# Kernel optimization log

Measured on AMD Instinct MI355X. Metric: run time of the kernel, lower is better.

## Reference

```python
import jax, jax.numpy as jnp
import numpy as np

N = 10000      # nodes
E = 160000     # edges (avg degree 16)
DIN = 512      # in_channels
H = 512        # hidden_channels
OUT = 128      # out_channels
L = 3          # num_layers
EPS_LN = 1e-5


def _ln(x):
    # F.layer_norm over last dim, no learned affine
    m = jnp.mean(x, axis=-1, keepdims=True)
    v = jnp.mean((x - m) ** 2, axis=-1, keepdims=True)
    return (x - m) * jax.lax.rsqrt(v + EPS_LN)


def setup_inputs() -> dict:
    key = jax.random.key(0)
    ks = jax.random.split(key, 16)
    s = 0.02
    return {
        "x": jax.random.normal(ks[0], (N, DIN), jnp.float32),
        "edge_index": jax.random.randint(ks[1], (2, E), 0, N, dtype=jnp.int64),
        "W_in": jax.random.normal(ks[2], (DIN, H), jnp.float32) * s,
        "b_in": jnp.zeros((H,), jnp.float32),
        "Wq": jax.random.normal(ks[3], (L, H, H), jnp.float32) * s,
        "Wk": jax.random.normal(ks[4], (L, H, H), jnp.float32) * s,
        "Wv": jax.random.normal(ks[5], (L, H, H), jnp.float32) * s,
        "Wo": jax.random.normal(ks[6], (L, H, H), jnp.float32) * s,
        "bo": jnp.zeros((L, H), jnp.float32),
        "W_gcn": jax.random.normal(ks[7], (H, H), jnp.float32) * s,
        "b_gcn": jnp.zeros((H,), jnp.float32),
        "W_mix": jax.random.normal(ks[8], (2 * H, H), jnp.float32) * s,
        "b_mix": jnp.zeros((H,), jnp.float32),
        "W_cls": jax.random.normal(ks[9], (H, OUT), jnp.float32) * s,
        "b_cls": jnp.zeros((OUT,), jnp.float32),
    }


def _attn_layer(x, wq, wk, wv, wo, bo):
    q = jax.nn.elu(x @ wq) + 1.0               # [N,H], positive feature map
    k = jax.nn.elu(x @ wk) + 1.0               # [N,H]
    v = x @ wv                                  # [N,H]
    kv = k.T @ v                                # [H,H]
    z = 1.0 / jnp.maximum(q @ k.sum(axis=0), 1e-6)   # [N]
    h = (q @ kv) * z[:, None]                   # [N,H]
    return h @ wo + bo


def _gcn(x, edge_index, w, b):
    # PyG GCNConv: x@W, add self-loops, symmetric D^-1/2 (A+I) D^-1/2, +bias
    xw = x @ w
    n = xw.shape[0]
    loops = jnp.arange(n, dtype=edge_index.dtype)
    src = jnp.concatenate([edge_index[0], loops])
    dst = jnp.concatenate([edge_index[1], loops])
    deg = jax.ops.segment_sum(jnp.ones_like(dst, jnp.float32), dst, num_segments=n)
    dis = jnp.where(deg > 0, jax.lax.rsqrt(jnp.maximum(deg, 1e-12)), 0.0)
    norm = dis[src] * dis[dst]                  # [E+N]
    msg = xw[src] * norm[:, None]               # [E+N,H]
    return jax.ops.segment_sum(msg, dst, num_segments=n) + b


def reference(x, edge_index, W_in, b_in, Wq, Wk, Wv, Wo, bo,
              W_gcn, b_gcn, W_mix, b_mix, W_cls, b_cls):
    # eval mode: dropout is identity
    x0 = jax.nn.relu(x @ W_in + b_in)           # [N,H]
    h_global = x0
    for i in range(Wq.shape[0]):
        h = _attn_layer(h_global, Wq[i], Wk[i], Wv[i], Wo[i], bo[i])
        h_global = _ln(h_global + h)
    h_graph = jax.nn.relu(_gcn(x0, edge_index, W_gcn, b_gcn))
    h = jax.nn.relu(jnp.concatenate([h_global, h_graph], axis=-1) @ W_mix + b_mix)
    return h @ W_cls + b_cls                    # [N,OUT]
```

## Files before the change

kernel.cpp:

```cpp
#include <hip/hip_runtime.h>
#include <hip/hip_bf16.h>

#define NNODES 10000
#define EEDGES 160000
#define HD     512
#define OUTD   128
#define NLAYERS 3
#define MP     10112
#define KTP    10240

#define ACT_NONE 0
#define ACT_RELU 1
#define ACT_ELU1 2

typedef __attribute__((ext_vector_type(8))) short bf16x8;
typedef __attribute__((ext_vector_type(4))) float f32x4;

__device__ __forceinline__ void gload16(const void* g, void* l) {
  __builtin_amdgcn_global_load_lds(
      (const __attribute__((address_space(1))) void*)g,
      (__attribute__((address_space(3))) void*)l, 16, 0, 0);
}

__device__ __forceinline__ void unp8(uint4 v, float* f) {
  const ushort* u = (const ushort*)&v;
#pragma unroll
  for (int j = 0; j < 8; ++j) f[j] = __uint_as_float(((unsigned)u[j]) << 16);
}

__device__ __forceinline__ ushort f2bu(float f) {
  __hip_bfloat16 h = __float2bfloat16(f);
  return *reinterpret_cast<ushort*>(&h);
}

__device__ __forceinline__ float elu1f(float v) {
  return (v > 0.f) ? (v + 1.0f) : __expf(v);
}

__global__ void fill_f32(float* p, float v, int n) {
  int i = blockIdx.x * blockDim.x + threadIdx.x;
  if (i < n) p[i] = v;
}
__global__ void fill_i32(int* p, int v, int n) {
  int i = blockIdx.x * blockDim.x + threadIdx.x;
  if (i < n) p[i] = v;
}

__global__ void probe_i64_k(const void* ei, int* flag, int E_) {
  int i = blockIdx.x * blockDim.x + threadIdx.x;
  if (i < E_) {
    if (((const int*)ei)[2 * i + 1] != 0) atomicOr(flag, 1);
  }
}
__device__ inline void load_edge(const void* ei, int is_i32, int e, int E_, int& s, int& d) {
  if (is_i32) { s = ((const int*)ei)[e]; d = ((const int*)ei)[E_ + e]; }
  else { s = (int)((const long long*)ei)[e]; d = (int)((const long long*)ei)[E_ + e]; }
}

template<int ACT, int HAS_BIAS, int HAS_SCALE, int OUTF, int OUTB, int ATOMIC, int TQKV>
__global__ __launch_bounds__(256) void mgemm(
    const __hip_bfloat16* __restrict__ A, const __hip_bfloat16* __restrict__ Bt,
    const float* __restrict__ bias, const float* __restrict__ rowscale,
    float* __restrict__ Cf, __hip_bfloat16* __restrict__ Cb,
    __hip_bfloat16* __restrict__ kTp, __hip_bfloat16* __restrict__ vTp,
    int M, int lda, int ldb, int ldc, int ldcb, int Ksz)
{
  __shared__ __align__(16) __hip_bfloat16 As[128 * 32];
  __shared__ __align__(16) __hip_bfloat16 Bs[128 * 32];
  __shared__ __align__(16) ushort eps[TQKV ? 128 * 136 : 8];

  int nwg = gridDim.x * gridDim.y;
  int orig = blockIdx.y * gridDim.x + blockIdx.x;
  int qq = nwg >> 3, rr8 = nwg & 7;
  int xcd = orig & 7, idx = orig >> 3;
  int wg = (xcd < rr8 ? xcd * (qq + 1) : rr8 * (qq + 1) + (xcd - rr8) * qq) + idx;
  int bx = wg % gridDim.x, by = wg / gridDim.x;

  int tid = threadIdx.x;
  int lane = tid & 63;
  int wave = tid >> 6;
  int wm = wave >> 1, wn = wave & 1;
  int row0 = by * 128;
  int col0 = bx * 128;
  int koff = blockIdx.z * Ksz;
  int srow = lane >> 2;
  int sbyte = (lane & 3) * 16;

  f32x4 acc[4][4];
#pragma unroll
  for (int i = 0; i < 4; ++i)
#pragma unroll
    for (int j = 0; j < 4; ++j) acc[i][j] = f32x4{0.f, 0.f, 0.f, 0.f};

  int r16 = lane & 15;
  int kg = (lane >> 4) * 16;

  for (int k0 = koff; k0 < koff + Ksz; k0 += 32) {
#pragma unroll
    for (int j = 0; j < 2; ++j) {
      int c = wave * 2 + j;
      const char* ga = (const char*)(A + (long)(row0 + c * 16 + srow) * lda + k0) + sbyte;
      gload16(ga, (char*)As + c * 1024);
      const char* gb = (const char*)(Bt + (long)(col0 + c * 16 + srow) * ldb + k0) + sbyte;
      gload16(gb, (char*)Bs + c * 1024);
    }
    __syncthreads();
    bf16x8 af[4], bfr[4];
#pragma unroll
    for (int i = 0; i < 4; ++i)
      af[i] = *(const bf16x8*)((const char*)As + (wm * 64 + i * 16 + r16) * 64 + kg);
#pragma unroll
    for (int i = 0; i < 4; ++i)
      bfr[i] = *(const bf16x8*)((const char*)Bs + (wn * 64 + i * 16 + r16) * 64 + kg);
#pragma unroll
    for (int i = 0; i < 4; ++i)
#pragma unroll
      for (int j = 0; j < 4; ++j)
        acc[i][j] = __builtin_amdgcn_mfma_f32_16x16x32_bf16(af[i], bfr[j], acc[i][j], 0, 0, 0);
    __syncthreads();
  }

  int rg = (lane >> 4) * 4;
  if (TQKV) {
    int colg = col0 + wn * 64;
    int g = colg >> 9;
    int cbase = col0 & 511;
#pragma unroll
    for (int i = 0; i < 4; ++i) {
#pragma unroll
      for (int j = 0; j < 4; ++j) {
        int c_l = wn * 64 + j * 16 + r16;
        int row_l = wm * 64 + i * 16 + rg;
        if (g == 0) {
#pragma unroll
          for (int r = 0; r < 4; ++r)
            eps[(row_l + r) * 136 + c_l] = f2bu(elu1f(acc[i][j][r]));
        } else {
          ushort4 o;
          o.x = f2bu(g == 1 ? elu1f(acc[i][j][0]) : acc[i][j][0]);
          o.y = f2bu(g == 1 ? elu1f(acc[i][j][1]) : acc[i][j][1]);
          o.z = f2bu(g == 1 ? elu1f(acc[i][j][2]) : acc[i][j][2]);
          o.w = f2bu(g == 1 ? elu1f(acc[i][j][3]) : acc[i][j][3]);
          *(ushort4*)&eps[c_l * 136 + row_l] = o;
        }
      }
    }
    __syncthreads();
    int l16 = tid & 15, cw = tid >> 4;
    if (g == 0) {
#pragma unroll
      for (int rr = cw; rr < 128; rr += 16) {
        int node = row0 + rr;
        if (node < NNODES)
          *(uint4*)((ushort*)Cb + (long)node * ldcb + cbase + l16 * 8) =
              *(const uint4*)&eps[rr * 136 + l16 * 8];
      }
    } else {
      ushort* T = (ushort*)(g == 1 ? kTp : vTp);
      int node0 = row0 + l16 * 8;
      if (node0 < NNODES) {
#pragma unroll
        for (int cc = cw; cc < 128; cc += 16)
          *(uint4*)(T + (long)(cbase + cc) * KTP + node0) = *(const uint4*)&eps[cc * 136 + l16 * 8];
      }
    }
    return;
  }
#pragma unroll
  for (int i = 0; i < 4; ++i) {
#pragma unroll
    for (int j = 0; j < 4; ++j) {
      int col = col0 + wn * 64 + j * 16 + r16;
#pragma unroll
      for (int r = 0; r < 4; ++r) {
        int row = row0 + wm * 64 + i * 16 + rg + r;
        if (row >= M) continue;
        float v = acc[i][j][r];
        if (ATOMIC) { atomicAdd(&Cf[(long)row * ldc + col], v); continue; }
        if (HAS_SCALE) v *= rowscale[row];
        if (HAS_BIAS) v += bias[col];
        if (ACT == ACT_RELU) v = fmaxf(v, 0.f);
        if (ACT == ACT_ELU1) v = elu1f(v);
        if (OUTF) Cf[(long)row * ldc + col] = v;
        if (OUTB) Cb[(long)row * ldcb + col] = __float2bfloat16(v);
      }
    }
  }
}

__global__ __launch_bounds__(256) void wtrans_k(
    const float* W_in, const float* Wq, const float* Wk, const float* Wv,
    const float* Wo, const float* W_gcn, const float* W_mix,
    __hip_bfloat16* WT, __hip_bfloat16* WMT)
{
  int z = blockIdx.z;
  const float* src;
  __hip_bfloat16* out;
  int ldout = 512, koff = 0;
  if (z == 0) { src = W_in; out = WT; }
  else if (z <= 9) {
    int l = (z - 1) / 3, w = (z - 1) % 3;
    src = (w == 0 ? Wq : w == 1 ? Wk : Wv) + (long)l * 262144;
    out = WT + (long)z * 262144;
  } else if (z <= 12) { src = Wo + (long)(z - 10) * 262144; out = WT + (long)z * 262144; }
  else if (z == 13) { src = W_gcn; out = WT + 13L * 262144; }
  else { src = W_mix + (long)(z - 14) * 262144; out = WMT; ldout = 1024; koff = (z - 14) * 512; }
  __shared__ float t[32][33];
  int r0 = blockIdx.y * 32, c0 = blockIdx.x * 32;
  int tx = threadIdx.x & 31, ty = threadIdx.x >> 5;
#pragma unroll
  for (int i = 0; i < 32; i += 8) t[ty + i][tx] = src[(long)(r0 + ty + i) * 512 + c0 + tx];
  __syncthreads();
#pragma unroll
  for (int i = 0; i < 32; i += 8)
    out[(long)(c0 + ty + i) * ldout + koff + r0 + tx] = __float2bfloat16(t[tx][ty + i]);
}

__global__ __launch_bounds__(256) void wtrans_cls_k(const float* Wc, __hip_bfloat16* out) {
  __shared__ float t[32][33];
  int r0 = blockIdx.y * 32, c0 = blockIdx.x * 32;
  int tx = threadIdx.x & 31, ty = threadIdx.x >> 5;
#pragma unroll
  for (int i = 0; i < 32; i += 8) t[ty + i][tx] = Wc[(long)(r0 + ty + i) * 128 + c0 + tx];
  __syncthreads();
#pragma unroll
  for (int i = 0; i < 32; i += 8)
    out[(long)(c0 + ty + i) * 512 + r0 + tx] = __float2bfloat16(t[tx][ty + i]);
}

__global__ void castx_k(const float* __restrict__ x, __hip_bfloat16* __restrict__ xb) {
  long i = (long)blockIdx.x * 256 + threadIdx.x;
  long base = i * 8;
  if (base >= (long)MP * HD) return;
  int row = (int)(base >> 9);
  ushort o[8];
  if (row < NNODES) {
    float4 a = *(const float4*)(x + base);
    float4 b = *(const float4*)(x + base + 4);
    float f[8] = {a.x, a.y, a.z, a.w, b.x, b.y, b.z, b.w};
#pragma unroll
    for (int j = 0; j < 8; ++j) o[j] = f2bu(f[j]);
  } else {
#pragma unroll
    for (int j = 0; j < 8; ++j) o[j] = 0;
  }
  *(uint4*)((ushort*)xb + base) = *(const uint4*)o;
}

__global__ __launch_bounds__(256) void pzcs_k(__hip_bfloat16* kT, __hip_bfloat16* vT,
                                              float* __restrict__ ksum) {
  int i = (blockIdx.x * 256 + threadIdx.x) >> 6;
  int lane = threadIdx.x & 63;
  ushort* kr = (ushort*)kT + (long)i * KTP;
  ushort* vr = (ushort*)vT + (long)i * KTP;
  if (lane < 60) {
    ushort4 z4 = {0, 0, 0, 0};
    *(ushort4*)(kr + NNODES + lane * 4) = z4;
    *(ushort4*)(vr + NNODES + lane * 4) = z4;
  }
  float s = 0.f;
  for (int off = lane * 8; off < NNODES; off += 512) {
    uint4 v = *(const uint4*)(kr + off);
    float f[8]; unp8(v, f);
#pragma unroll
    for (int j = 0; j < 8; ++j) s += f[j];
  }
#pragma unroll
  for (int o = 32; o > 0; o >>= 1) s += __shfl_down(s, o);
  if (lane == 0) ksum[i] = s;
}

__global__ __launch_bounds__(256) void z_k(const __hip_bfloat16* __restrict__ qb,
                                           const float* __restrict__ ksum, float* __restrict__ z) {
  long gid = (long)blockIdx.x * 256 + threadIdx.x;
  int row = (int)(gid >> 6), lane = (int)(gid & 63);
  if (row >= NNODES) return;
  uint4 qv = *(const uint4*)((const ushort*)qb + (long)row * HD + lane * 8);
  float f[8]; unp8(qv, f);
  const float* kk = ksum + lane * 8;
  float s = 0.f;
#pragma unroll
  for (int j = 0; j < 8; ++j) s += f[j] * kk[j];
#pragma unroll
  for (int o = 32; o > 0; o >>= 1) s += __shfl_down(s, o);
  if (lane == 0) z[row] = 1.0f / fmaxf(s, 1e-6f);
}

__global__ void cast8_k(const float* __restrict__ s, __hip_bfloat16* __restrict__ d, int n8) {
  int i = blockIdx.x * 256 + threadIdx.x;
  if (i >= n8) return;
  float4 a = ((const float4*)s)[2 * i], b = ((const float4*)s)[2 * i + 1];
  float f[8] = {a.x, a.y, a.z, a.w, b.x, b.y, b.z, b.w};
  ushort o[8];
#pragma unroll
  for (int j = 0; j < 8; ++j) o[j] = f2bu(f[j]);
  *(uint4*)((ushort*)d + (long)i * 8) = *(const uint4*)o;
}

__global__ __launch_bounds__(256) void ln_res_k(float* __restrict__ hg,
                                                const __hip_bfloat16* __restrict__ hb,
                                                __hip_bfloat16* __restrict__ hgcat) {
  int wid = (blockIdx.x * 256 + threadIdx.x) >> 6;
  int lane = threadIdx.x & 63;
  if (wid >= NNODES) return;
  float* row = hg + (long)wid * HD + lane * 8;
  uint4 hv = *(const uint4*)((const ushort*)hb + (long)wid * HD + lane * 8);
  float hf[8]; unp8(hv, hf);
  float4 p0 = *(const float4*)row, p1 = *(const float4*)(row + 4);
  float a[8] = {p0.x + hf[0], p0.y + hf[1], p0.z + hf[2], p0.w + hf[3],
                p1.x + hf[4], p1.y + hf[5], p1.z + hf[6], p1.w + hf[7]};
  float s = 0.f;
#pragma unroll
  for (int j = 0; j < 8; ++j) s += a[j];
#pragma unroll
  for (int o = 1; o < 64; o <<= 1) s += __shfl_xor(s, o);
  float mean = s * (1.0f / HD);
  float vs = 0.f;
#pragma unroll
  for (int j = 0; j < 8; ++j) { a[j] -= mean; vs += a[j] * a[j]; }
#pragma unroll
  for (int o = 1; o < 64; o <<= 1) vs += __shfl_xor(vs, o);
  float inv = rsqrtf(vs * (1.0f / HD) + 1e-5f);
  ushort ob[8];
#pragma unroll
  for (int j = 0; j < 8; ++j) { a[j] *= inv; ob[j] = f2bu(a[j]); }
  *(float4*)row = make_float4(a[0], a[1], a[2], a[3]);
  *(float4*)(row + 4) = make_float4(a[4], a[5], a[6], a[7]);
  *(uint4*)((ushort*)hgcat + (long)wid * 1024 + lane * 8) = *(const uint4*)ob;
}

__global__ void cnt_k(const void* ei, const int* flag, int* cnt, int E_) {
  int e = blockIdx.x * blockDim.x + threadIdx.x;
  if (e >= E_) return;
  int s, d; load_edge(ei, *flag, e, E_, s, d);
  atomicAdd(&cnt[d], 1);
}
__global__ __launch_bounds__(256) void scan_k(const int* __restrict__ cnt, int* __restrict__ rowptr,
                                              int* __restrict__ cursor, float* __restrict__ dis) {
  __shared__ int ps[256];
  int t = threadIdx.x;
  int lo = t * 40, hi = min(lo + 40, NNODES);
  int s = 0;
  for (int i = lo; i < hi; ++i) s += cnt[i];
  ps[t] = s;
  __syncthreads();
  for (int o = 1; o < 256; o <<= 1) {
    int v = (t >= o) ? ps[t - o] : 0;
    __syncthreads();
    ps[t] += v;
    __syncthreads();
  }
  int run = (t == 0) ? 0 : ps[t - 1];
  for (int i = lo; i < hi; ++i) {
    rowptr[i] = run; cursor[i] = run;
    dis[i] = rsqrtf((float)cnt[i] + 1.0f);
    run += cnt[i];
  }
  if (t == 255) rowptr[NNODES] = run;
}
__global__ void csrfill_k(const void* ei, const int* flag, int* cursor, int* csr, int E_) {
  int e = blockIdx.x * blockDim.x + threadIdx.x;
  if (e >= E_) return;
  int s, d; load_edge(ei, *flag, e, E_, s, d);
  int pos = atomicAdd(&cursor[d], 1);
  csr[pos] = s;
}
__global__ __launch_bounds__(256) void gcn_gather_k(
    const __hip_bfloat16* __restrict__ xwb, const int* __restrict__ rowptr,
    const int* __restrict__ csr, const float* __restrict__ dis,
    const float* __restrict__ bgcn, __hip_bfloat16* __restrict__ hgcat)
{
  int wid = (blockIdx.x * 256 + threadIdx.x) >> 6;
  int lane = threadIdx.x & 63;
  if (wid >= NNODES) return;
  int d = wid;
  float dd = dis[d];
  float acc[8], f[8];
  uint4 v = *(const uint4*)((const ushort*)xwb + (long)d * HD + lane * 8);
  unp8(v, f);
#pragma unroll
  for (int j = 0; j < 8; ++j) acc[j] = f[j] * dd * dd;
  int e0 = rowptr[d], e1 = rowptr[d + 1];
  for (int e = e0; e < e1; ++e) {
    int sN = csr[e];
    float w = dis[sN] * dd;
    uint4 xv = *(const uint4*)((const ushort*)xwb + (long)sN * HD + lane * 8);
    unp8(xv, f);
#pragma unroll
    for (int j = 0; j < 8; ++j) acc[j] = fmaf(f[j], w, acc[j]);
  }
  const float* bb = bgcn + lane * 8;
  ushort o[8];
#pragma unroll
  for (int j = 0; j < 8; ++j) o[j] = f2bu(fmaxf(acc[j] + bb[j], 0.f));
  *(uint4*)((ushort*)hgcat + (long)d * 1024 + 512 + lane * 8) = *(const uint4*)o;
}

extern "C" void kernel_launch(void* const* d_in, const int* in_sizes, int n_in,
                              void* d_out, int out_size, void* d_ws, size_t ws_size,
                              hipStream_t stream) {
  const float* x     = (const float*)d_in[0];
  const void*  ei    = d_in[1];
  const float* W_in  = (const float*)d_in[2];
  const float* b_in  = (const float*)d_in[3];
  const float* Wq    = (const float*)d_in[4];
  const float* Wk    = (const float*)d_in[5];
  const float* Wv    = (const float*)d_in[6];
  const float* Wo    = (const float*)d_in[7];
  const float* bo    = (const float*)d_in[8];
  const float* W_gcn = (const float*)d_in[9];
  const float* b_gcn = (const float*)d_in[10];
  const float* W_mix = (const float*)d_in[11];
  const float* b_mix = (const float*)d_in[12];
  const float* W_cls = (const float*)d_in[13];
  const float* b_cls = (const float*)d_in[14];
  float* out = (float*)d_out;

  char* p = (char*)d_ws;
  __hip_bfloat16* WT  = (__hip_bfloat16*)p; p += 14L * 262144 * 2;
  __hip_bfloat16* WMT = (__hip_bfloat16*)p; p += 512L * 1024 * 2;
  __hip_bfloat16* WCT = (__hip_bfloat16*)p; p += 128L * 512 * 2;
  float* hg = (float*)p; p += (long)MP * HD * 4;
  __hip_bfloat16* hgcat = (__hip_bfloat16*)p; p += (long)MP * 1024 * 2;
  __hip_bfloat16* qb = (__hip_bfloat16*)p; p += (long)MP * HD * 2;
  __hip_bfloat16* vT = (__hip_bfloat16*)p; p += 512L * KTP * 2;
  __hip_bfloat16* kT = (__hip_bfloat16*)p; p += 512L * KTP * 2;
  float* kvf = (float*)p; p += 512L * 512 * 4;
  __hip_bfloat16* kvb  = (__hip_bfloat16*)p; p += 512L * 512 * 2;
  __hip_bfloat16* kvoT = (__hip_bfloat16*)p; p += 512L * 512 * 2;
  float* ksum = (float*)p; p += 2048;
  float* zb   = (float*)p; p += (long)MP * 4;
  int* cnt    = (int*)p; p += 40000;
  int* rowptr = (int*)p; p += 40016;
  int* cursor = (int*)p; p += 40000;
  float* dis  = (float*)p; p += 40000;
  int* csr    = (int*)p; p += 640000;
  int* flag   = (int*)p; p += 4;

  __hip_bfloat16* xb    = qb;
  __hip_bfloat16* xwb   = qb;
  __hip_bfloat16* hb    = kT;
  __hip_bfloat16* hmixb = kT;

  dim3 blk(256);
  dim3 gG(4, MP / 128);
  dim3 gQKV(12, MP / 128);
  dim3 gKV(4, 4, 16);
  dim3 gS(4, 4);
  dim3 gCls(1, MP / 128);

  wtrans_k<<<dim3(16, 16, 16), blk, 0, stream>>>(W_in, Wq, Wk, Wv, Wo, W_gcn, W_mix, WT, WMT);
  wtrans_cls_k<<<dim3(4, 16), blk, 0, stream>>>(W_cls, WCT);
  castx_k<<<(int)(((long)MP * HD / 8 + 255) / 256), blk, 0, stream>>>(x, xb);
  fill_i32<<<1, 1, 0, stream>>>(flag, 0, 1);
  probe_i64_k<<<(EEDGES + 255) / 256, 256, 0, stream>>>(ei, flag, EEDGES);

  mgemm<ACT_RELU, 1, 0, 1, 1, 0, 0><<<gG, blk, 0, stream>>>(
      xb, WT, b_in, nullptr, hg, hgcat, nullptr, nullptr, NNODES, HD, HD, HD, 1024, HD);

  mgemm<ACT_NONE, 0, 0, 0, 1, 0, 0><<<gG, blk, 0, stream>>>(
      hgcat, WT + 13L * 262144, nullptr, nullptr, nullptr, xwb, nullptr, nullptr,
      NNODES, 1024, HD, HD, HD, HD);
  fill_i32<<<40, 256, 0, stream>>>(cnt, 0, NNODES);
  cnt_k<<<(EEDGES + 255) / 256, 256, 0, stream>>>(ei, flag, cnt, EEDGES);
  scan_k<<<1, 256, 0, stream>>>(cnt, rowptr, cursor, dis);
  csrfill_k<<<(EEDGES + 255) / 256, 256, 0, stream>>>(ei, flag, cursor, csr, EEDGES);
  gcn_gather_k<<<2500, blk, 0, stream>>>(xwb, rowptr, csr, dis, b_gcn, hgcat);

  for (int l = 0; l < NLAYERS; ++l) {
    const __hip_bfloat16* BtQKV = WT + (long)(1 + 3 * l) * 262144;
    const __hip_bfloat16* WoT   = WT + (long)(10 + l) * 262144;

    mgemm<ACT_NONE, 0, 0, 0, 0, 0, 1><<<gQKV, blk, 0, stream>>>(
        hgcat, BtQKV, nullptr, nullptr, nullptr, qb, kT, vT,
        NNODES, 1024, HD, HD, HD, HD);
    pzcs_k<<<128, blk, 0, stream>>>(kT, vT, ksum);

    fill_f32<<<1024, 256, 0, stream>>>(kvf, 0.f, HD * HD);
    mgemm<ACT_NONE, 0, 0, 0, 0, 1, 0><<<gKV, blk, 0, stream>>>(
        kT, vT, nullptr, nullptr, kvf, nullptr, nullptr, nullptr,
        HD, KTP, KTP, HD, HD, 640);
    cast8_k<<<128, blk, 0, stream>>>(kvf, kvb, HD * HD / 8);

    mgemm<ACT_NONE, 0, 0, 0, 1, 0, 0><<<gS, blk, 0, stream>>>(
        WoT, kvb, nullptr, nullptr, nullptr, kvoT, nullptr, nullptr,
        HD, HD, HD, HD, HD, HD);

    z_k<<<2500, blk, 0, stream>>>(qb, ksum, zb);
    mgemm<ACT_NONE, 1, 1, 0, 1, 0, 0><<<gG, blk, 0, stream>>>(
        qb, kvoT, bo + (long)l * HD, zb, nullptr, hb, nullptr, nullptr,
        NNODES, HD, HD, HD, HD, HD);
    ln_res_k<<<2500, blk, 0, stream>>>(hg, hb, hgcat);
  }

  mgemm<ACT_RELU, 1, 0, 0, 1, 0, 0><<<gG, blk, 0, stream>>>(
      hgcat, WMT, b_mix, nullptr, nullptr, hmixb, nullptr, nullptr,
      NNODES, 1024, 1024, HD, HD, 1024);
  mgemm<ACT_NONE, 1, 0, 1, 0, 0, 0><<<gCls, blk, 0, stream>>>(
      hmixb, WCT, b_cls, nullptr, out, nullptr, nullptr, nullptr,
      NNODES, HD, HD, OUTD, OUTD, HD);
}
```

Baseline: 731.0 us.

## Fuse init fills, column-sum k in QKV epilogue, merge weight transposes

Replaces the separate fill kernels with one init kernel that zeroes per-layer kv accumulators, ksum, counts, flag and the kT/vT padding up front. The column sum of k is now computed in the QKV GEMM epilogue with wave shuffles and atomics, which removes the per-layer pzcs kernel and its reread of kT. It also folds the W_cls transpose into wtrans_k, uses a ballot in the int64 probe to cut atomics, and unrolls the GCN gather by two edges. Together these remove several launches and memory passes, at the cost of atomics in the GEMM epilogue and an accumulation order that is no longer deterministic.

Result: faster. 703.3 us (-3.8%).

```diff
diff --git a/kernel.cpp b/kernel.cpp
--- a/kernel.cpp
+++ b/kernel.cpp
@@ -37,20 +37,32 @@
   return (v > 0.f) ? (v + 1.0f) : __expf(v);
 }
 
-__global__ void fill_f32(float* p, float v, int n) {
-  int i = blockIdx.x * blockDim.x + threadIdx.x;
-  if (i < n) p[i] = v;
-}
-__global__ void fill_i32(int* p, int v, int n) {
-  int i = blockIdx.x * blockDim.x + threadIdx.x;
-  if (i < n) p[i] = v;
+__global__ __launch_bounds__(256) void init_k(int* cnt, int* flag, float* ksum,
+                                              float* kvf, __hip_bfloat16* kT,
+                                              __hip_bfloat16* vT) {
+  int i = blockIdx.x * 256 + threadIdx.x;
+  if (i < 3 * HD * HD) { kvf[i] = 0.f; return; }
+  i -= 3 * HD * HD;
+  if (i < NNODES) { cnt[i] = 0; return; }
+  i -= NNODES;
+  if (i < 3 * HD) { ksum[i] = 0.f; return; }
+  i -= 3 * HD;
+  if (i == 0) { *flag = 0; return; }
+  i -= 1;
+  if (i < 512 * 120 * 2) {
+    int b = i / (512 * 120);
+    int r = (i % (512 * 120)) / 120;
+    int c = (i % 120);
+    uint* T = (uint*)(b == 0 ? kT : vT);
+    T[((long)r * KTP + NNODES) / 2 + c] = 0u;
+  }
 }
 
 __global__ void probe_i64_k(const void* ei, int* flag, int E_) {
   int i = blockIdx.x * blockDim.x + threadIdx.x;
-  if (i < E_) {
-    if (((const int*)ei)[2 * i + 1] != 0) atomicOr(flag, 1);
-  }
+  bool nz = (i < E_) && (((const int*)ei)[2 * i + 1] != 0);
+  unsigned long long m = __ballot(nz);
+  if ((threadIdx.x & 63) == 0 && m) atomicOr(flag, 1);
 }
 __device__ inline void load_edge(const void* ei, int is_i32, int e, int E_, int& s, int& d) {
   if (is_i32) { s = ((const int*)ei)[e]; d = ((const int*)ei)[E_ + e]; }
@@ -125,6 +137,24 @@
     int colg = col0 + wn * 64;
     int g = colg >> 9;
     int cbase = col0 & 511;
+    if (g == 1) {
+#pragma unroll
+      for (int j = 0; j < 4; ++j) {
+        float cs = 0.f;
+#pragma unroll
+        for (int i = 0; i < 4; ++i) {
+          int rowbase = row0 + wm * 64 + i * 16 + rg;
+          if (rowbase < NNODES) {
+#pragma unroll
+            for (int r = 0; r < 4; ++r) cs += elu1f(acc[i][j][r]);
+          }
+        }
+        cs += __shfl_xor(cs, 16);
+        cs += __shfl_xor(cs, 32);
+        if ((lane >> 4) == 0)
+          atomicAdd(&Cf[cbase + wn * 64 + j * 16 + r16], cs);
+      }
+    }
 #pragma unroll
     for (int i = 0; i < 4; ++i) {
 #pragma unroll
@@ -190,13 +220,13 @@
 
 __global__ __launch_bounds__(256) void wtrans_k(
     const float* W_in, const float* Wq, const float* Wk, const float* Wv,
-    const float* Wo, const float* W_gcn, const float* W_mix,
-    __hip_bfloat16* WT, __hip_bfloat16* WMT)
+    const float* Wo, const float* W_gcn, const float* W_mix, const float* W_cls,
+    __hip_bfloat16* WT, __hip_bfloat16* WMT, __hip_bfloat16* WCT)
 {
   int z = blockIdx.z;
   const float* src;
   __hip_bfloat16* out;
-  int ldout = 512, koff = 0;
+  int ldout = 512, koff = 0, ldsrc = 512;
   if (z == 0) { src = W_in; out = WT; }
   else if (z <= 9) {
     int l = (z - 1) / 3, w = (z - 1) % 3;
@@ -204,28 +234,20 @@
     out = WT + (long)z * 262144;
   } else if (z <= 12) { src = Wo + (long)(z - 10) * 262144; out = WT + (long)z * 262144; }
   else if (z == 13) { src = W_gcn; out = WT + 13L * 262144; }
-  else { src = W_mix + (long)(z - 14) * 262144; out = WMT; ldout = 1024; koff = (z - 14) * 512; }
+  else if (z <= 15) { src = W_mix + (long)(z - 14) * 262144; out = WMT; ldout = 1024; koff = (z - 14) * 512; }
+  else {
+    if (blockIdx.x >= 4) return;
+    src = W_cls; out = WCT; ldsrc = 128;
+  }
   __shared__ float t[32][33];
   int r0 = blockIdx.y * 32, c0 = blockIdx.x * 32;
   int tx = threadIdx.x & 31, ty = threadIdx.x >> 5;
 #pragma unroll
-  for (int i = 0; i < 32; i += 8) t[ty + i][tx] = src[(long)(r0 + ty + i) * 512 + c0 + tx];
+  for (int i = 0; i < 32; i += 8) t[ty + i][tx] = src[(long)(r0 + ty + i) * ldsrc + c0 + tx];
   __syncthreads();
 #pragma unroll
   for (int i = 0; i < 32; i += 8)
     out[(long)(c0 + ty + i) * ldout + koff + r0 + tx] = __float2bfloat16(t[tx][ty + i]);
-}
-
-__global__ __launch_bounds__(256) void wtrans_cls_k(const float* Wc, __hip_bfloat16* out) {
-  __shared__ float t[32][33];
-  int r0 = blockIdx.y * 32, c0 = blockIdx.x * 32;
-  int tx = threadIdx.x & 31, ty = threadIdx.x >> 5;
-#pragma unroll
-  for (int i = 0; i < 32; i += 8) t[ty + i][tx] = Wc[(long)(r0 + ty + i) * 128 + c0 + tx];
-  __syncthreads();
-#pragma unroll
-  for (int i = 0; i < 32; i += 8)
-    out[(long)(c0 + ty + i) * 512 + r0 + tx] = __float2bfloat16(t[tx][ty + i]);
 }
 
 __global__ void castx_k(const float* __restrict__ x, __hip_bfloat16* __restrict__ xb) {
@@ -245,29 +267,6 @@
     for (int j = 0; j < 8; ++j) o[j] = 0;
   }
   *(uint4*)((ushort*)xb + base) = *(const uint4*)o;
-}
-
-__global__ __launch_bounds__(256) void pzcs_k(__hip_bfloat16* kT, __hip_bfloat16* vT,
-                                              float* __restrict__ ksum) {
-  int i = (blockIdx.x * 256 + threadIdx.x) >> 6;
-  int lane = threadIdx.x & 63;
-  ushort* kr = (ushort*)kT + (long)i * KTP;
-  ushort* vr = (ushort*)vT + (long)i * KTP;
-  if (lane < 60) {
-    ushort4 z4 = {0, 0, 0, 0};
-    *(ushort4*)(kr + NNODES + lane * 4) = z4;
-    *(ushort4*)(vr + NNODES + lane * 4) = z4;
-  }
-  float s = 0.f;
-  for (int off = lane * 8; off < NNODES; off += 512) {
-    uint4 v = *(const uint4*)(kr + off);
-    float f[8]; unp8(v, f);
-#pragma unroll
-    for (int j = 0; j < 8; ++j) s += f[j];
-  }
-#pragma unroll
-  for (int o = 32; o > 0; o >>= 1) s += __shfl_down(s, o);
-  if (lane == 0) ksum[i] = s;
 }
 
 __global__ __launch_bounds__(256) void z_k(const __hip_bfloat16* __restrict__ qb,
@@ -375,13 +374,23 @@
   if (wid >= NNODES) return;
   int d = wid;
   float dd = dis[d];
-  float acc[8], f[8];
+  float acc[8], f[8], f2[8];
   uint4 v = *(const uint4*)((const ushort*)xwb + (long)d * HD + lane * 8);
   unp8(v, f);
 #pragma unroll
   for (int j = 0; j < 8; ++j) acc[j] = f[j] * dd * dd;
   int e0 = rowptr[d], e1 = rowptr[d + 1];
-  for (int e = e0; e < e1; ++e) {
+  int e = e0;
+  for (; e + 1 < e1; e += 2) {
+    int s0 = csr[e], s1 = csr[e + 1];
+    float w0 = dis[s0] * dd, w1 = dis[s1] * dd;
+    uint4 xv0 = *(const uint4*)((const ushort*)xwb + (long)s0 * HD + lane * 8);
+    uint4 xv1 = *(const uint4*)((const ushort*)xwb + (long)s1 * HD + lane * 8);
+    unp8(xv0, f); unp8(xv1, f2);
+#pragma unroll
+    for (int j = 0; j < 8; ++j) acc[j] = fmaf(f[j], w0, fmaf(f2[j], w1, acc[j]));
+  }
+  if (e < e1) {
     int sN = csr[e];
     float w = dis[sN] * dd;
     uint4 xv = *(const uint4*)((const ushort*)xwb + (long)sN * HD + lane * 8);
@@ -425,10 +434,10 @@
   __hip_bfloat16* qb = (__hip_bfloat16*)p; p += (long)MP * HD * 2;
   __hip_bfloat16* vT = (__hip_bfloat16*)p; p += 512L * KTP * 2;
   __hip_bfloat16* kT = (__hip_bfloat16*)p; p += 512L * KTP * 2;
-  float* kvf = (float*)p; p += 512L * 512 * 4;
+  float* kvf = (float*)p; p += 3L * 512 * 512 * 4;
   __hip_bfloat16* kvb  = (__hip_bfloat16*)p; p += 512L * 512 * 2;
   __hip_bfloat16* kvoT = (__hip_bfloat16*)p; p += 512L * 512 * 2;
-  float* ksum = (float*)p; p += 2048;
+  float* ksum = (float*)p; p += 3L * 512 * 4;
   float* zb   = (float*)p; p += (long)MP * 4;
   int* cnt    = (int*)p; p += 40000;
   int* rowptr = (int*)p; p += 40016;
@@ -449,10 +458,13 @@
   dim3 gS(4, 4);
   dim3 gCls(1, MP / 128);
 
-  wtrans_k<<<dim3(16, 16, 16), blk, 0, stream>>>(W_in, Wq, Wk, Wv, Wo, W_gcn, W_mix, WT, WMT);
-  wtrans_cls_k<<<dim3(4, 16), blk, 0, stream>>>(W_cls, WCT);
+  {
+    int initN = 3 * HD * HD + NNODES + 3 * HD + 1 + 512 * 120 * 2;
+    init_k<<<(initN + 255) / 256, blk, 0, stream>>>(cnt, flag, ksum, kvf, kT, vT);
+  }
+  wtrans_k<<<dim3(16, 16, 17), blk, 0, stream>>>(W_in, Wq, Wk, Wv, Wo, W_gcn, W_mix,
+                                                 W_cls, WT, WMT, WCT);
   castx_k<<<(int)(((long)MP * HD / 8 + 255) / 256), blk, 0, stream>>>(x, xb);
-  fill_i32<<<1, 1, 0, stream>>>(flag, 0, 1);
   probe_i64_k<<<(EEDGES + 255) / 256, 256, 0, stream>>>(ei, flag, EEDGES);
 
   mgemm<ACT_RELU, 1, 0, 1, 1, 0, 0><<<gG, blk, 0, stream>>>(
@@ -461,7 +473,6 @@
   mgemm<ACT_NONE, 0, 0, 0, 1, 0, 0><<<gG, blk, 0, stream>>>(
       hgcat, WT + 13L * 262144, nullptr, nullptr, nullptr, xwb, nullptr, nullptr,
       NNODES, 1024, HD, HD, HD, HD);
-  fill_i32<<<40, 256, 0, stream>>>(cnt, 0, NNODES);
   cnt_k<<<(EEDGES + 255) / 256, 256, 0, stream>>>(ei, flag, cnt, EEDGES);
   scan_k<<<1, 256, 0, stream>>>(cnt, rowptr, cursor, dis);
   csrfill_k<<<(EEDGES + 255) / 256, 256, 0, stream>>>(ei, flag, cursor, csr, EEDGES);
@@ -470,23 +481,23 @@
   for (int l = 0; l < NLAYERS; ++l) {
     const __hip_bfloat16* BtQKV = WT + (long)(1 + 3 * l) * 262144;
     const __hip_bfloat16* WoT   = WT + (long)(10 + l) * 262144;
+    float* kvfl  = kvf + (long)l * HD * HD;
+    float* ksuml = ksum + (long)l * HD;
 
     mgemm<ACT_NONE, 0, 0, 0, 0, 0, 1><<<gQKV, blk, 0, stream>>>(
-        hgcat, BtQKV, nullptr, nullptr, nullptr, qb, kT, vT,
+        hgcat, BtQKV, nullptr, nullptr, ksuml, qb, kT, vT,
         NNODES, 1024, HD, HD, HD, HD);
-    pzcs_k<<<128, blk, 0, stream>>>(kT, vT, ksum);
-
-    fill_f32<<<1024, 256, 0, stream>>>(kvf, 0.f, HD * HD);
+
     mgemm<ACT_NONE, 0, 0, 0, 0, 1, 0><<<gKV, blk, 0, stream>>>(
-        kT, vT, nullptr, nullptr, kvf, nullptr, nullptr, nullptr,
+        kT, vT, nullptr, nullptr, kvfl, nullptr, nullptr, nullptr,
         HD, KTP, KTP, HD, HD, 640);
-    cast8_k<<<128, blk, 0, stream>>>(kvf, kvb, HD * HD / 8);
+    cast8_k<<<128, blk, 0, stream>>>(kvfl, kvb, HD * HD / 8);
 
     mgemm<ACT_NONE, 0, 0, 0, 1, 0, 0><<<gS, blk, 0, stream>>>(
         WoT, kvb, nullptr, nullptr, nullptr, kvoT, nullptr, nullptr,
         HD, HD, HD, HD, HD, HD);
 
-    z_k<<<2500, blk, 0, stream>>>(qb, ksum, zb);
+    z_k<<<2500, blk, 0, stream>>>(qb, ksuml, zb);
     mgemm<ACT_NONE, 1, 1, 0, 1, 0, 0><<<gG, blk, 0, stream>>>(
         qb, kvoT, bo + (long)l * HD, zb, nullptr, hb, nullptr, nullptr,
         NNODES, HD, HD, HD, HD, HD);
```
